# Performance work log

Measured on AMD Instinct MI355X. Metric: run time of the kernel, lower is better.

## Reference

```python
import jax, jax.numpy as jnp
import numpy as np

N_NODES = 100000
N_EDGES = 800000
D_IN = 128
D_HID = 128
D_OUT = 128
NUM_GRAPHS = 64


def gcn_conv(x, src, dst, W, b, n_nodes):
    """PyG GCNConv: h = D^{-1/2} (A + I) D^{-1/2} (x W) + b, with self-loops included in src/dst."""
    h = x @ W  # [N, d_out]
    deg = jax.ops.segment_sum(jnp.ones_like(dst, dtype=h.dtype), dst, num_segments=n_nodes)
    dinv = jnp.where(deg > 0, jax.lax.rsqrt(deg), 0.0)
    norm = dinv[src] * dinv[dst]  # [E]
    out = jax.ops.segment_sum(h[src] * norm[:, None], dst, num_segments=n_nodes)
    return out + b


def setup_inputs() -> dict:
    key = jax.random.key(0)
    ks = jax.random.split(key, 10)
    x = jax.random.normal(ks[0], (N_NODES, D_IN), dtype=jnp.float32)
    edge_index = jax.random.randint(ks[1], (2, N_EDGES), 0, N_NODES, dtype=jnp.int64)
    batch = jnp.sort(jax.random.randint(ks[2], (N_NODES,), 0, NUM_GRAPHS, dtype=jnp.int64))
    s1 = 1.0 / np.sqrt(D_IN)
    s2 = 1.0 / np.sqrt(D_HID)
    W1 = jax.random.uniform(ks[3], (D_IN, D_HID), jnp.float32, -s1, s1)
    b1 = jnp.zeros((D_HID,), jnp.float32)
    W2 = jax.random.uniform(ks[4], (D_HID, D_HID), jnp.float32, -s2, s2)
    b2 = jnp.zeros((D_HID,), jnp.float32)
    Wfc = jax.random.uniform(ks[5], (D_HID, D_OUT), jnp.float32, -s2, s2)
    bfc = jax.random.uniform(ks[6], (D_OUT,), jnp.float32, -s2, s2)
    return {"x": x, "edge_index": edge_index, "batch": batch,
            "W1": W1, "b1": b1, "W2": W2, "b2": b2, "Wfc": Wfc, "bfc": bfc}


def reference(x, edge_index, batch, W1, b1, W2, b2, Wfc, bfc):
    n = x.shape[0]
    loop = jnp.arange(n, dtype=edge_index.dtype)
    src = jnp.concatenate([edge_index[0], loop])
    dst = jnp.concatenate([edge_index[1], loop])
    h = jax.nn.relu(gcn_conv(x, src, dst, W1, b1, n))
    h = jax.nn.relu(gcn_conv(h, src, dst, W2, b2, n))
    # global_mean_pool over graph ids
    sums = jax.ops.segment_sum(h, batch, num_segments=NUM_GRAPHS)
    cnts = jax.ops.segment_sum(jnp.ones((n,), h.dtype), batch, num_segments=NUM_GRAPHS)
    pooled = sums / jnp.maximum(cnts, 1.0)[:, None]
    return pooled @ Wfc + bfc
```

## Files before the change

### kernel.cpp

```cpp
#include <hip/hip_runtime.h>
#include <hip/hip_bf16.h>

#define N_NODES 100000
#define N_EDGES 800000
#define D 128
#define NG 64
#define SCAN_NB ((N_NODES + 255) / 256)
#define NTILES ((N_NODES + 63) / 64)

typedef __attribute__((ext_vector_type(8))) short short8;
typedef __attribute__((ext_vector_type(4))) float f32x4;
typedef __attribute__((ext_vector_type(2))) float f32x2;

static __device__ __forceinline__ unsigned short f2bf(float f) {
    unsigned u = __float_as_uint(f);
    unsigned r = (u + 0x7FFF + ((u >> 16) & 1)) >> 16;
    return (unsigned short)r;
}
static __device__ __forceinline__ float bf2f(unsigned short b) {
    return __uint_as_float((unsigned)b << 16);
}
static __device__ __forceinline__ unsigned char f2fp8(float v) {
    int p = __builtin_amdgcn_cvt_pk_fp8_f32(v, v, 0, false);
    return (unsigned char)(p & 0xFF);
}
static __device__ __forceinline__ f32x2 fp8x2_f32(unsigned short s) {
    return __builtin_amdgcn_cvt_pk_f32_fp8((int)s, false);
}


__global__ void hist_kernel(const int* __restrict__ dst, int* __restrict__ deg) {
    int e = blockIdx.x * blockDim.x + threadIdx.x;
    if (e < N_EDGES) atomicAdd(&deg[dst[e]], 1);
}

__global__ __launch_bounds__(256) void scan1_kernel(const int* __restrict__ deg,
                                                    int* __restrict__ rs,
                                                    int* __restrict__ bsum,
                                                    float* __restrict__ dinv) {
    __shared__ int wsum[4];
    int i = blockIdx.x * 256 + threadIdx.x;
    int lane = threadIdx.x & 63;
    int wid = threadIdx.x >> 6;
    int v = (i < N_NODES) ? deg[i] : 0;
    if (i < N_NODES) dinv[i] = rsqrtf((float)v + 1.0f);
    int x = v;
    #pragma unroll
    for (int off = 1; off < 64; off <<= 1) {
        int y = __shfl_up(x, off);
        if (lane >= off) x += y;
    }
    if (lane == 63) wsum[wid] = x;
    __syncthreads();
    int add = 0;
    #pragma unroll
    for (int w = 0; w < 3; ++w) if (w < wid) add += wsum[w];
    int incl = x + add;
    if (i < N_NODES) rs[i] = incl - v;
    if (threadIdx.x == 255) bsum[blockIdx.x] = incl;
}

__global__ __launch_bounds__(512) void scan2_kernel(int* __restrict__ bsum) {
    __shared__ int s[512];
    int t = threadIdx.x;
    int v = (t < SCAN_NB) ? bsum[t] : 0;
    s[t] = v;
    __syncthreads();
    for (int off = 1; off < 512; off <<= 1) {
        int y = (t >= off) ? s[t - off] : 0;
        __syncthreads();
        s[t] += y;
        __syncthreads();
    }
    if (t < SCAN_NB) bsum[t] = s[t] - v;
}

__global__ void scan3_kernel(int* __restrict__ rs, const int* __restrict__ bsum) {
    int i = blockIdx.x * blockDim.x + threadIdx.x;
    if (i < N_NODES) rs[i] += bsum[i >> 8];
    if (i == 0) rs[N_NODES] = N_EDGES;
}

__global__ void fill_kernel(const int* __restrict__ src, const int* __restrict__ dst,
                            const float* __restrict__ dinv, const int* __restrict__ rs,
                            int* __restrict__ cursor, int2* __restrict__ pairs) {
    int e = blockIdx.x * blockDim.x + threadIdx.x;
    if (e < N_EDGES) {
        int d = dst[e];
        int s = src[e];
        int p = rs[d] + atomicAdd(&cursor[d], 1);
        pairs[p] = make_int2(s, __float_as_int(dinv[s] * dinv[d]));
    }
}


__global__ void bounds_kernel(const int* __restrict__ batch, int* __restrict__ start) {
    int g = threadIdx.x;
    if (g > NG) return;
    if (g == NG) { start[NG] = N_NODES; return; }
    int lo = 0, hi = N_NODES;
    while (lo < hi) {
        int mid = (lo + hi) >> 1;
        if (batch[mid] < g) lo = mid + 1; else hi = mid;
    }
    start[g] = lo;
}


template <bool IN_F32>
__global__ __launch_bounds__(512) void xw_mfma_kernel(const void* __restrict__ Xin,
                                                      const float* __restrict__ W,
                                                      unsigned char* __restrict__ Hq) {
    __shared__ __align__(16) unsigned short bt_hi[128 * 128];
    __shared__ __align__(16) unsigned short bt_lo[128 * 128];
    __shared__ __align__(16) unsigned short atile[64 * 128];

    const int t = threadIdx.x;
    const int lane = t & 63;
    const int wid = t >> 6;

    #pragma unroll 4
    for (int i = 0; i < 32; ++i) {
        int idx = t + i * 512;
        int k = idx >> 7;
        int n = idx & 127;
        float w = W[idx];
        unsigned short hi = f2bf(w);
        unsigned short lo = f2bf(w - bf2f(hi));
        int byte = (n * 256 + k * 2) ^ ((n & 7) << 4);
        *(unsigned short*)((char*)bt_hi + byte) = hi;
        *(unsigned short*)((char*)bt_lo + byte) = lo;
    }

    const int mrow = (wid >> 1) * 16;
    const int ncol = (wid & 1) * 64;
    const int ar = mrow + (lane & 15);
    const int ak = (lane >> 4) * 8;

    for (int tile = blockIdx.x; tile < NTILES; tile += gridDim.x) {
        const int node0 = tile * 64;
        __syncthreads();

        #pragma unroll
        for (int p = 0; p < 2; ++p) {
            int j = t + p * 512;
            int row = j >> 4;
            int c8 = (j & 15) * 8;
            int node = node0 + row;
            short8 v = 0;
            if (IN_F32) {
                const float* X = (const float*)Xin;
                if (node < N_NODES) {
                    const float* xr = &X[(size_t)node * 128 + c8];
                    float4 a = *(const float4*)xr;
                    float4 b = *(const float4*)(xr + 4);
                    v[0] = (short)f2bf(a.x); v[1] = (short)f2bf(a.y);
                    v[2] = (short)f2bf(a.z); v[3] = (short)f2bf(a.w);
                    v[4] = (short)f2bf(b.x); v[5] = (short)f2bf(b.y);
                    v[6] = (short)f2bf(b.z); v[7] = (short)f2bf(b.w);
                }
            } else {
                const unsigned short* X = (const unsigned short*)Xin;
                if (node < N_NODES) v = *(const short8*)&X[(size_t)node * 128 + c8];
            }
            int byte = (row * 256 + c8 * 2) ^ ((row & 7) << 4);
            *(short8*)((char*)atile + byte) = v;
        }
        __syncthreads();

        f32x4 acc[4];
        #pragma unroll
        for (int nt = 0; nt < 4; ++nt) acc[nt] = 0.f;

        #pragma unroll
        for (int kc = 0; kc < 128; kc += 32) {
            short8 a = *(const short8*)((const char*)atile +
                        ((ar * 256 + (kc + ak) * 2) ^ ((ar & 7) << 4)));
            #pragma unroll
            for (int nt = 0; nt < 4; ++nt) {
                int col = ncol + nt * 16 + (lane & 15);
                int boff = (col * 256 + (kc + ak) * 2) ^ ((col & 7) << 4);
                short8 bh = *(const short8*)((const char*)bt_hi + boff);
                acc[nt] = __builtin_amdgcn_mfma_f32_16x16x32_bf16(a, bh, acc[nt], 0, 0, 0);
                short8 bl = *(const short8*)((const char*)bt_lo + boff);
                acc[nt] = __builtin_amdgcn_mfma_f32_16x16x32_bf16(a, bl, acc[nt], 0, 0, 0);
            }
        }

        #pragma unroll
        for (int nt = 0; nt < 4; ++nt) {
            #pragma unroll
            for (int r = 0; r < 4; ++r) {
                int node = node0 + mrow + (lane >> 4) * 4 + r;
                if (node < N_NODES)
                    Hq[(size_t)node * 128 + ncol + nt * 16 + (lane & 15)] = f2fp8(acc[nt][r]);
            }
        }
    }
}


__global__ __launch_bounds__(256) void gather_kernel(const unsigned char* __restrict__ Hq,
                                                     const int* __restrict__ rs,
                                                     const int2* __restrict__ pairs,
                                                     const float* __restrict__ dinv,
                                                     const float* __restrict__ bias,
                                                     unsigned short* __restrict__ out) {
    int node = blockIdx.x * 4 + (threadIdx.x >> 6);
    if (node >= N_NODES) return;
    int lane = threadIdx.x & 63;

    float di = dinv[node];
    unsigned short sv = *(const unsigned short*)&Hq[(size_t)node * 128 + lane * 2];
    f32x2 hs = fp8x2_f32(sv);
    float2 bb = *(const float2*)&bias[lane * 2];
    float ax = hs[0] * di * di + bb.x;
    float ay = hs[1] * di * di + bb.y;

    int beg = rs[node];
    int end = rs[node + 1];
    if (end > beg) {
        int last = end - 1;
        for (int i = beg; i < end; i += 8) {
            #pragma unroll
            for (int j = 0; j < 8; ++j) {
                int idx = i + j;
                int2 p = pairs[min(idx, last)];
                float w = (idx < end) ? __int_as_float(p.y) : 0.f;
                unsigned short hv = *(const unsigned short*)&Hq[(size_t)p.x * 128 + lane * 2];
                f32x2 hf = fp8x2_f32(hv);
                ax = fmaf(hf[0], w, ax);
                ay = fmaf(hf[1], w, ay);
            }
        }
    }
    ushort2 o;
    o.x = f2bf(fmaxf(ax, 0.f));
    o.y = f2bf(fmaxf(ay, 0.f));
    *(ushort2*)&out[(size_t)node * 128 + lane * 2] = o;
}


__global__ __launch_bounds__(256) void pool_kernel(const unsigned short* __restrict__ G,
                                                   const int* __restrict__ start,
                                                   float* __restrict__ sums) {
    __shared__ float red[16][132];
    int g = blockIdx.x >> 4;
    int s = blockIdx.x & 15;
    int n0 = start[g], n1 = start[g + 1];
    int slot = threadIdx.x & 15;
    int nl = threadIdx.x >> 4;

    float acc[8];
    #pragma unroll
    for (int j = 0; j < 8; ++j) acc[j] = 0.f;

    for (int node = n0 + s * 16 + nl; node < n1; node += 256) {
        short8 v = *(const short8*)&G[(size_t)node * 128 + slot * 8];
        #pragma unroll
        for (int j = 0; j < 8; ++j) acc[j] += bf2f((unsigned short)v[j]);
    }

    #pragma unroll
    for (int j = 0; j < 8; ++j) red[nl][slot * 8 + j] = acc[j];
    __syncthreads();
    #pragma unroll
    for (int off = 8; off > 0; off >>= 1) {
        if (nl < off) {
            #pragma unroll
            for (int j = 0; j < 8; ++j)
                red[nl][slot * 8 + j] += red[nl + off][slot * 8 + j];
        }
        __syncthreads();
    }
    if (nl == 0) {
        #pragma unroll
        for (int j = 0; j < 8; ++j)
            unsafeAtomicAdd(&sums[g * D + slot * 8 + j], red[0][slot * 8 + j]);
    }
}


__global__ void fc_kernel(const float* __restrict__ sums, const int* __restrict__ start,
                          const float* __restrict__ Wfc, const float* __restrict__ bfc,
                          float* __restrict__ out) {
    __shared__ __align__(16) float ps[D];
    int g = blockIdx.x;
    int f = threadIdx.x;
    float c = (float)max(start[g + 1] - start[g], 1);
    ps[f] = sums[g * D + f] / c;
    __syncthreads();
    float acc = bfc[f];
    #pragma unroll
    for (int k = 0; k < D; k += 4) {
        float4 pv = *(const float4*)&ps[k];
        acc += pv.x * Wfc[k * D + f] + pv.y * Wfc[(k + 1) * D + f] +
               pv.z * Wfc[(k + 2) * D + f] + pv.w * Wfc[(k + 3) * D + f];
    }
    out[g * D + f] = acc;
}

extern "C" void kernel_launch(void* const* d_in, const int* in_sizes, int n_in,
                              void* d_out, int out_size, void* d_ws, size_t ws_size,
                              hipStream_t stream) {
    const float* x   = (const float*)d_in[0];
    const int* ei    = (const int*)d_in[1];
    const int* batch = (const int*)d_in[2];
    const float* W1  = (const float*)d_in[3];
    const float* b1  = (const float*)d_in[4];
    const float* W2  = (const float*)d_in[5];
    const float* b2  = (const float*)d_in[6];
    const float* Wfc = (const float*)d_in[7];
    const float* bfc = (const float*)d_in[8];
    float* out = (float*)d_out;

    const int* src = ei;
    const int* dst = ei + N_EDGES;

    unsigned char* Hq    = (unsigned char*)d_ws;
    unsigned short* G    = (unsigned short*)(Hq + (size_t)N_NODES * D);
    int2* pairs          = (int2*)(G + (size_t)N_NODES * D);
    float* dinv          = (float*)(pairs + N_EDGES);
    int*   deg           = (int*)(dinv + N_NODES);
    int*   cursor        = deg + N_NODES;
    int*   rs            = cursor + N_NODES;
    int*   bsum          = rs + N_NODES + 4;
    int*   start         = bsum + 512;
    float* sums          = (float*)(start + NG + 8);

    hipMemsetAsync(deg, 0, 2 * N_NODES * sizeof(int), stream);
    hipMemsetAsync(sums, 0, NG * D * sizeof(float), stream);

    hist_kernel<<<(N_EDGES + 255) / 256, 256, 0, stream>>>(dst, deg);
    scan1_kernel<<<SCAN_NB, 256, 0, stream>>>(deg, rs, bsum, dinv);
    scan2_kernel<<<1, 512, 0, stream>>>(bsum);
    scan3_kernel<<<SCAN_NB, 256, 0, stream>>>(rs, bsum);
    fill_kernel<<<(N_EDGES + 255) / 256, 256, 0, stream>>>(src, dst, dinv, rs, cursor, pairs);
    bounds_kernel<<<1, 128, 0, stream>>>(batch, start);

    xw_mfma_kernel<true><<<512, 512, 0, stream>>>(x, W1, Hq);
    gather_kernel<<<(N_NODES + 3) / 4, 256, 0, stream>>>(Hq, rs, pairs, dinv, b1, G);

    xw_mfma_kernel<false><<<512, 512, 0, stream>>>(G, W2, Hq);
    gather_kernel<<<(N_NODES + 3) / 4, 256, 0, stream>>>(Hq, rs, pairs, dinv, b2, G);

    pool_kernel<<<NG * 16, 256, 0, stream>>>(G, start, sums);
    fc_kernel<<<NG, 128, 0, stream>>>(sums, start, Wfc, bfc, out);
}
```

Baseline: 374.9 us.

## Split each wavefront into four edge groups with 8-byte fp8 row loads

The gather kernel now splits each 64-lane wavefront into four 16-lane groups. Each group handles a different neighbour edge and loads 8 fp8 features per lane as one 8-byte read, where before the whole wave walked edges one at a time with 2-byte loads. The partial sums are combined with cross-group xor shuffles, and one group adds bias, applies ReLU and writes 16-byte bf16 outputs. This raises memory-level parallelism and load width per edge, at the cost of more shuffles and more registers, and partially empty groups on low-degree nodes.

```diff
diff --git a/kernel.cpp b/kernel.cpp
--- a/kernel.cpp
+++ b/kernel.cpp
@@ -23,9 +23,6 @@
 static __device__ __forceinline__ unsigned char f2fp8(float v) {
     int p = __builtin_amdgcn_cvt_pk_fp8_f32(v, v, 0, false);
     return (unsigned char)(p & 0xFF);
-}
-static __device__ __forceinline__ f32x2 fp8x2_f32(unsigned short s) {
-    return __builtin_amdgcn_cvt_pk_f32_fp8((int)s, false);
 }
 
 
@@ -209,35 +206,63 @@
     int node = blockIdx.x * 4 + (threadIdx.x >> 6);
     if (node >= N_NODES) return;
     int lane = threadIdx.x & 63;
+    int g = lane >> 4;
+    int fl = lane & 15;
 
     float di = dinv[node];
-    unsigned short sv = *(const unsigned short*)&Hq[(size_t)node * 128 + lane * 2];
-    f32x2 hs = fp8x2_f32(sv);
-    float2 bb = *(const float2*)&bias[lane * 2];
-    float ax = hs[0] * di * di + bb.x;
-    float ay = hs[1] * di * di + bb.y;
+    float wself = (g == 0) ? di * di : 0.f;
+
+    float acc[8];
+    {
+        uint2 sv = *(const uint2*)&Hq[(size_t)node * 128 + fl * 8];
+        f32x2 a0 = __builtin_amdgcn_cvt_pk_f32_fp8((int)sv.x, false);
+        f32x2 a1 = __builtin_amdgcn_cvt_pk_f32_fp8((int)sv.x, true);
+        f32x2 a2 = __builtin_amdgcn_cvt_pk_f32_fp8((int)sv.y, false);
+        f32x2 a3 = __builtin_amdgcn_cvt_pk_f32_fp8((int)sv.y, true);
+        acc[0] = a0[0] * wself; acc[1] = a0[1] * wself;
+        acc[2] = a1[0] * wself; acc[3] = a1[1] * wself;
+        acc[4] = a2[0] * wself; acc[5] = a2[1] * wself;
+        acc[6] = a3[0] * wself; acc[7] = a3[1] * wself;
+    }
 
     int beg = rs[node];
     int end = rs[node + 1];
-    if (end > beg) {
-        int last = end - 1;
-        for (int i = beg; i < end; i += 8) {
-            #pragma unroll
-            for (int j = 0; j < 8; ++j) {
-                int idx = i + j;
-                int2 p = pairs[min(idx, last)];
-                float w = (idx < end) ? __int_as_float(p.y) : 0.f;
-                unsigned short hv = *(const unsigned short*)&Hq[(size_t)p.x * 128 + lane * 2];
-                f32x2 hf = fp8x2_f32(hv);
-                ax = fmaf(hf[0], w, ax);
-                ay = fmaf(hf[1], w, ay);
-            }
-        }
-    }
-    ushort2 o;
-    o.x = f2bf(fmaxf(ax, 0.f));
-    o.y = f2bf(fmaxf(ay, 0.f));
-    *(ushort2*)&out[(size_t)node * 128 + lane * 2] = o;
+    int last = end - 1;
+    for (int i = beg; i < end; i += 4) {
+        int idx = i + g;
+        int2 p = pairs[min(idx, last)];
+        float w = (idx < end) ? __int_as_float(p.y) : 0.f;
+        uint2 hv = *(const uint2*)&Hq[(size_t)p.x * 128 + fl * 8];
+        f32x2 h0 = __builtin_amdgcn_cvt_pk_f32_fp8((int)hv.x, false);
+        f32x2 h1 = __builtin_amdgcn_cvt_pk_f32_fp8((int)hv.x, true);
+        f32x2 h2 = __builtin_amdgcn_cvt_pk_f32_fp8((int)hv.y, false);
+        f32x2 h3 = __builtin_amdgcn_cvt_pk_f32_fp8((int)hv.y, true);
+        acc[0] = fmaf(h0[0], w, acc[0]); acc[1] = fmaf(h0[1], w, acc[1]);
+        acc[2] = fmaf(h1[0], w, acc[2]); acc[3] = fmaf(h1[1], w, acc[3]);
+        acc[4] = fmaf(h2[0], w, acc[4]); acc[5] = fmaf(h2[1], w, acc[5]);
+        acc[6] = fmaf(h3[0], w, acc[6]); acc[7] = fmaf(h3[1], w, acc[7]);
+    }
+
+    #pragma unroll
+    for (int mask = 16; mask <= 32; mask <<= 1) {
+        #pragma unroll
+        for (int j = 0; j < 8; ++j) acc[j] += __shfl_xor(acc[j], mask);
+    }
+
+    if (g == 0) {
+        float4 bb0 = *(const float4*)&bias[fl * 8];
+        float4 bb1 = *(const float4*)&bias[fl * 8 + 4];
+        short8 o;
+        o[0] = (short)f2bf(fmaxf(acc[0] + bb0.x, 0.f));
+        o[1] = (short)f2bf(fmaxf(acc[1] + bb0.y, 0.f));
+        o[2] = (short)f2bf(fmaxf(acc[2] + bb0.z, 0.f));
+        o[3] = (short)f2bf(fmaxf(acc[3] + bb0.w, 0.f));
+        o[4] = (short)f2bf(fmaxf(acc[4] + bb1.x, 0.f));
+        o[5] = (short)f2bf(fmaxf(acc[5] + bb1.y, 0.f));
+        o[6] = (short)f2bf(fmaxf(acc[6] + bb1.z, 0.f));
+        o[7] = (short)f2bf(fmaxf(acc[7] + bb1.w, 0.f));
+        *(short8*)&out[(size_t)node * 128 + fl * 8] = o;
+    }
 }
 
 
```

After: 324.7 us. 1.15x faster.
